# Kernel optimization log

Measured on AMD Instinct MI355X. Metric: run time of the kernel, lower is better.

Reference implementation:

```python
import jax, jax.numpy as jnp
import numpy as np

N_NODES = 100000


def _sage_conv(x, src, dst, w_l, b_l, w_r):
    # PyG SAGEConv (mean aggr): out = lin_l(mean_{j in N(i)} x_j) + lin_r(x_i)
    msg = x[src]                                   # [E, d] gather
    agg = jax.ops.segment_sum(msg, dst, num_segments=N_NODES)   # [N, d]
    deg = jax.ops.segment_sum(jnp.ones_like(dst, dtype=x.dtype), dst,
                              num_segments=N_NODES)             # [N]
    mean = agg / jnp.maximum(deg, 1.0)[:, None]
    return mean @ w_l.T + b_l + x @ w_r.T


def setup_inputs() -> dict:
    key = jax.random.key(0)
    ks = jax.random.split(key, 8)
    in_dim, hid, out_dim = 128, 128, 64
    n_edges = 1600000
    x = jax.random.normal(ks[0], (N_NODES, in_dim), dtype=jnp.float32)
    edge_index = jax.random.randint(ks[1], (2, n_edges), 0, N_NODES, dtype=jnp.int64)
    s1 = 1.0 / np.sqrt(in_dim)
    s2 = 1.0 / np.sqrt(hid)
    w1_l = jax.random.uniform(ks[2], (hid, in_dim), jnp.float32, -s1, s1)
    b1 = jax.random.uniform(ks[3], (hid,), jnp.float32, -s1, s1)
    w1_r = jax.random.uniform(ks[4], (hid, in_dim), jnp.float32, -s1, s1)
    w2_l = jax.random.uniform(ks[5], (out_dim, hid), jnp.float32, -s2, s2)
    b2 = jax.random.uniform(ks[6], (out_dim,), jnp.float32, -s2, s2)
    w2_r = jax.random.uniform(ks[7], (out_dim, hid), jnp.float32, -s2, s2)
    return {"x": x, "edge_index": edge_index, "w1_l": w1_l, "b1": b1,
            "w1_r": w1_r, "w2_l": w2_l, "b2": b2, "w2_r": w2_r}


def reference(x, edge_index, w1_l, b1, w1_r, w2_l, b2, w2_r):
    src, dst = edge_index[0], edge_index[1]
    h = _sage_conv(x, src, dst, w1_l, b1, w1_r)    # [N, hid]
    h = jax.nn.relu(h)
    out = _sage_conv(h, src, dst, w2_l, b2, w2_r)  # [N, out_dim]
    return out
```

## Files before the change

### kernel.cpp

```cpp
#include <hip/hip_runtime.h>


namespace {
constexpr int NN   = 100000;
constexpr int NE   = 1600000;
constexpr int NBKT = 391;
constexpr int PB   = 256;
constexpr int CE   = NE / PB;

constexpr size_t W_BKT  = 0;
constexpr size_t W_BASE = 400;
constexpr size_t W_BCUR = 800;
constexpr size_t W_OFF  = 1200;
constexpr size_t W_PART = 101616;
constexpr size_t W_CSR  = 1701616;
constexpr size_t W_B1   = 3301616;
constexpr size_t W_B2   = 3318000;
constexpr size_t W_XQ   = 3326192;
constexpr size_t W_XR   = 6526192;
constexpr size_t W_H    = 12926192;
constexpr size_t W_HL   = 19326192;
constexpr size_t W_HR   = 22526192;
}

using short8  = __attribute__((ext_vector_type(8)))  short;
using f32x16  = __attribute__((ext_vector_type(16))) float;
using floatx2 = __attribute__((ext_vector_type(2)))  float;

__device__ inline unsigned short f2b(float f) {
  unsigned u = __builtin_bit_cast(unsigned, f);
  u = (u + 0x7fffu + ((u >> 16) & 1u)) >> 16;
  return (unsigned short)u;
}
__device__ inline float b2f_lo(unsigned u) { return __builtin_bit_cast(float, u << 16); }
__device__ inline float b2f_hi(unsigned u) { return __builtin_bit_cast(float, u & 0xffff0000u); }
__device__ inline float b2f(unsigned short s) { return __builtin_bit_cast(float, ((unsigned)s) << 16); }


__global__ __launch_bounds__(256) void prebucket_k(const int* __restrict__ dst,
                                                   int* __restrict__ bktCnt) {
  __shared__ int h[NBKT];
  int t = threadIdx.x;
  for (int j = t; j < NBKT; j += 256) h[j] = 0;
  __syncthreads();
  const int base = blockIdx.x * CE;
  for (int i = t; i < CE; i += 256) atomicAdd(&h[dst[base + i] >> 8], 1);
  __syncthreads();
  for (int j = t; j < NBKT; j += 256) if (h[j]) atomicAdd(&bktCnt[j], h[j]);
}

__global__ __launch_bounds__(512) void scanb_k(const int* __restrict__ bktCnt,
                                               int* __restrict__ bktBase,
                                               int* __restrict__ bktCur) {
  __shared__ int s[512];
  int t = threadIdx.x;
  int v = (t < NBKT) ? bktCnt[t] : 0;
  s[t] = v;
  __syncthreads();
  #pragma unroll
  for (int d = 1; d < 512; d <<= 1) {
    int u = (t >= d) ? s[t - d] : 0;
    __syncthreads();
    s[t] += u;
    __syncthreads();
  }
  int excl = s[t] - v;
  if (t <= NBKT) bktBase[t] = excl;
  if (t < NBKT)  bktCur[t]  = excl;
}

__global__ __launch_bounds__(256) void partition_k(const int* __restrict__ src,
                                                   const int* __restrict__ dst,
                                                   int* __restrict__ bktCur,
                                                   int* __restrict__ part) {
  __shared__ int  hist[NBKT + 1];
  __shared__ int  lo[NBKT + 1];
  __shared__ int  cur[NBKT + 1];
  __shared__ int  gb[NBKT + 1];
  __shared__ int  sh[256];
  __shared__ int  stage[CE];
  __shared__ unsigned short sbkt[CE];
  int t = threadIdx.x;
  const int base = blockIdx.x * CE;

  for (int j = t; j < NBKT + 1; j += 256) hist[j] = 0;
  __syncthreads();
  for (int i = t; i < CE; i += 256) atomicAdd(&hist[dst[base + i] >> 8], 1);
  __syncthreads();

  int j0 = 2 * t, j1 = 2 * t + 1;
  int h0 = (j0 < NBKT) ? hist[j0] : 0;
  int h1 = (j1 < NBKT) ? hist[j1] : 0;
  int ps = h0 + h1;
  sh[t] = ps;
  __syncthreads();
  #pragma unroll
  for (int d = 1; d < 256; d <<= 1) {
    int u = (t >= d) ? sh[t - d] : 0;
    __syncthreads();
    sh[t] += u;
    __syncthreads();
  }
  int e0 = sh[t] - ps;
  if (j0 < NBKT + 1) { lo[j0] = e0; cur[j0] = e0; }
  if (j1 < NBKT + 1) { lo[j1] = e0 + h0; cur[j1] = e0 + h0; }
  __syncthreads();

  for (int i = t; i < CE; i += 256) {
    int d = dst[base + i], s = src[base + i];
    int b = d >> 8;
    int p = atomicAdd(&cur[b], 1);
    stage[p] = ((d & 255) << 23) | s;
    sbkt[p]  = (unsigned short)b;
  }
  __syncthreads();

  for (int j = t; j < NBKT; j += 256)
    gb[j] = hist[j] ? atomicAdd(&bktCur[j], hist[j]) : 0;
  __syncthreads();

  for (int i = t; i < CE; i += 256) {
    int b = sbkt[i];
    part[gb[b] + (i - lo[b])] = stage[i];
  }
}

__global__ __launch_bounds__(256) void cfill_k(const int* __restrict__ part,
                                               const int* __restrict__ bktBase,
                                               int* __restrict__ off,
                                               int* __restrict__ csr) {
  __shared__ int cnt[256];
  __shared__ int cur[256];
  __shared__ int sh[256];
  int t = threadIdx.x;
  const int b = blockIdx.x;
  const int beg = bktBase[b], end = bktBase[b + 1];

  cnt[t] = 0;
  __syncthreads();
  for (int i = beg + t; i < end; i += 256)
    atomicAdd(&cnt[((unsigned)part[i]) >> 23], 1);
  __syncthreads();

  int v = cnt[t];
  sh[t] = v;
  __syncthreads();
  #pragma unroll
  for (int d = 1; d < 256; d <<= 1) {
    int u = (t >= d) ? sh[t - d] : 0;
    __syncthreads();
    sh[t] += u;
    __syncthreads();
  }
  int excl = sh[t] - v;
  off[b * 256 + t] = beg + excl;
  cur[t] = excl;
  __syncthreads();

  for (int i = beg + t; i < end; i += 256) {
    int w = part[i];
    int j = ((unsigned)w) >> 23;
    int p = atomicAdd(&cur[j], 1);
    csr[beg + p] = w & 0x7FFFFF;
  }
}


__global__ void prep_b_k(const float* __restrict__ w1l, const float* __restrict__ w1r,
                         const float* __restrict__ w2l, const float* __restrict__ w2r,
                         unsigned short* __restrict__ b1p, unsigned short* __restrict__ b2p) {
  int e = blockIdx.x * blockDim.x + threadIdx.x;
  if (e >= 6144) return;
  bool g2 = e >= 4096;
  int le = g2 ? e - 4096 : e;
  int nf = le >> 9, kk = (le >> 6) & 7, l = le & 63;
  int n = nf * 32 + (l & 31), half = l >> 5;
  const float* Wlo = g2 ? w2l : w1l;
  const float* Whi = g2 ? w2r : w1r;
  int split = g2 ? 64 : 128;
  unsigned short o[8];
  #pragma unroll
  for (int j = 0; j < 8; ++j) {
    int k = kk * 16 + ((j >= 4) ? 8 : 0) + half * 4 + (j & 3);
    float v = (n < split) ? Wlo[(size_t)n * 128 + k] : Whi[(size_t)(n - split) * 128 + k];
    o[j] = f2b(v);
  }
  unsigned short* dstp = (g2 ? b2p : b1p) + (size_t)le * 8;
  *(short8*)dstp = __builtin_bit_cast(short8, *(const ulonglong2*)o);
}


template<int NCOLS, bool AFP32, int MODE>
__global__ __launch_bounds__(512, 2) void gemm_k(const void* __restrict__ Aptr, int M,
                                                 const unsigned short* __restrict__ Bpack,
                                                 void* __restrict__ Cv,
                                                 void* __restrict__ C2v) {
  constexpr int NF = NCOLS / 64;
  __shared__ unsigned short As[128 * 128];
  const int t  = threadIdx.x;
  const int m0 = blockIdx.x * 128;

  #pragma unroll
  for (int i = 0; i < 4; ++i) {
    int G = t + 512 * i;
    int r = G >> 4, g = G & 15;
    int m = m0 + r;
    short8 v = {0, 0, 0, 0, 0, 0, 0, 0};
    if (AFP32) {
      if (m < M) {
        const float* p = (const float*)Aptr + (size_t)m * 128 + g * 8;
        float4 a = *(const float4*)p;
        float4 b = *(const float4*)(p + 4);
        v[0] = (short)f2b(a.x); v[1] = (short)f2b(a.y);
        v[2] = (short)f2b(a.z); v[3] = (short)f2b(a.w);
        v[4] = (short)f2b(b.x); v[5] = (short)f2b(b.y);
        v[6] = (short)f2b(b.z); v[7] = (short)f2b(b.w);
      }
    } else {
      if (m < M) v = *(const short8*)((const unsigned short*)Aptr + (size_t)m * 128 + g * 8);
    }
    *(short8*)(As + r * 128 + ((g ^ (r & 15)) << 3)) = v;
  }
  __syncthreads();

  const int wid = t >> 6, lane = t & 63;
  const int mw = wid >> 1, nw = wid & 1;
  const int m = mw * 32 + (lane & 31), half = lane >> 5;

  short8 af[8];
  #pragma unroll
  for (int kk = 0; kk < 8; ++kk) {
    const unsigned* p0 = (const unsigned*)(As + m * 128 + (((2 * kk)     ^ (m & 15)) << 3) + half * 4);
    const unsigned* p1 = (const unsigned*)(As + m * 128 + (((2 * kk + 1) ^ (m & 15)) << 3) + half * 4);
    uint4 comb = make_uint4(p0[0], p0[1], p1[0], p1[1]);
    af[kk] = __builtin_bit_cast(short8, comb);
  }

  #pragma unroll
  for (int nf = 0; nf < NF; ++nf) {
    const int nfg = nw * NF + nf;
    f32x16 acc;
    #pragma unroll
    for (int i = 0; i < 16; ++i) acc[i] = 0.f;
    #pragma unroll
    for (int kk = 0; kk < 8; ++kk) {
      short8 bf = *(const short8*)(Bpack + ((size_t)((nfg * 8 + kk) * 64 + lane)) * 8);
      acc = __builtin_amdgcn_mfma_f32_32x32x16_bf16(af[kk], bf, acc, 0, 0, 0);
    }
    const int col = nfg * 32 + (lane & 31);
    #pragma unroll
    for (int q = 0; q < 4; ++q)
      #pragma unroll
      for (int rr = 0; rr < 4; ++rr) {
        int row = rr + 8 * q + 4 * half;
        int mo  = m0 + mw * 32 + row;
        if (mo < M) {
          float v = acc[q * 4 + rr];
          if (MODE == 1) {
            if (col < 128) {
              int p8 = __builtin_amdgcn_cvt_pk_fp8_f32(v, v, 0, false);
              ((unsigned char*)C2v)[(size_t)mo * 128 + col] = (unsigned char)(p8 & 0xff);
            } else {
              ((unsigned short*)Cv)[(size_t)mo * 128 + (col - 128)] = f2b(v);
            }
          } else {
            if (col < 64) {
              int p8 = __builtin_amdgcn_cvt_pk_fp8_f32(v, v, 0, false);
              ((unsigned char*)Cv)[(size_t)mo * 64 + col] = (unsigned char)(p8 & 0xff);
            } else {
              ((unsigned short*)C2v)[(size_t)mo * 64 + (col - 64)] = f2b(v);
            }
          }
        }
      }
  }
}


__global__ __launch_bounds__(256) void agg1_k(const unsigned char* __restrict__ xq,
                                              const unsigned short* __restrict__ xr,
                                              const int* __restrict__ off,
                                              const int* __restrict__ csr,
                                              const float* __restrict__ b1,
                                              unsigned short* __restrict__ h) {
  int wid  = (blockIdx.x * blockDim.x + threadIdx.x) >> 6;
  int lane = threadIdx.x & 63;
  if (wid >= NN) return;
  const int g = lane >> 4, sub = lane & 15;
  int s0 = off[wid], s1 = off[wid + 1];

  float acc[8];
  #pragma unroll
  for (int k = 0; k < 8; ++k) acc[k] = 0.f;

  for (int e = s0; e < s1; e += 16) {
    int e0 = e + g, e1 = e + 4 + g, e2 = e + 8 + g, e3 = e + 12 + g;
    uint2 v0 = make_uint2(0u, 0u), v1 = make_uint2(0u, 0u);
    uint2 v2 = make_uint2(0u, 0u), v3 = make_uint2(0u, 0u);
    if (e0 < s1) v0 = *(const uint2*)(xq + (size_t)csr[e0] * 128 + sub * 8);
    if (e1 < s1) v1 = *(const uint2*)(xq + (size_t)csr[e1] * 128 + sub * 8);
    if (e2 < s1) v2 = *(const uint2*)(xq + (size_t)csr[e2] * 128 + sub * 8);
    if (e3 < s1) v3 = *(const uint2*)(xq + (size_t)csr[e3] * 128 + sub * 8);
    floatx2 f;
    f = __builtin_amdgcn_cvt_pk_f32_fp8(v0.x, false); acc[0] += f.x; acc[1] += f.y;
    f = __builtin_amdgcn_cvt_pk_f32_fp8(v0.x, true);  acc[2] += f.x; acc[3] += f.y;
    f = __builtin_amdgcn_cvt_pk_f32_fp8(v0.y, false); acc[4] += f.x; acc[5] += f.y;
    f = __builtin_amdgcn_cvt_pk_f32_fp8(v0.y, true);  acc[6] += f.x; acc[7] += f.y;
    f = __builtin_amdgcn_cvt_pk_f32_fp8(v1.x, false); acc[0] += f.x; acc[1] += f.y;
    f = __builtin_amdgcn_cvt_pk_f32_fp8(v1.x, true);  acc[2] += f.x; acc[3] += f.y;
    f = __builtin_amdgcn_cvt_pk_f32_fp8(v1.y, false); acc[4] += f.x; acc[5] += f.y;
    f = __builtin_amdgcn_cvt_pk_f32_fp8(v1.y, true);  acc[6] += f.x; acc[7] += f.y;
    f = __builtin_amdgcn_cvt_pk_f32_fp8(v2.x, false); acc[0] += f.x; acc[1] += f.y;
    f = __builtin_amdgcn_cvt_pk_f32_fp8(v2.x, true);  acc[2] += f.x; acc[3] += f.y;
    f = __builtin_amdgcn_cvt_pk_f32_fp8(v2.y, false); acc[4] += f.x; acc[5] += f.y;
    f = __builtin_amdgcn_cvt_pk_f32_fp8(v2.y, true);  acc[6] += f.x; acc[7] += f.y;
    f = __builtin_amdgcn_cvt_pk_f32_fp8(v3.x, false); acc[0] += f.x; acc[1] += f.y;
    f = __builtin_amdgcn_cvt_pk_f32_fp8(v3.x, true);  acc[2] += f.x; acc[3] += f.y;
    f = __builtin_amdgcn_cvt_pk_f32_fp8(v3.y, false); acc[4] += f.x; acc[5] += f.y;
    f = __builtin_amdgcn_cvt_pk_f32_fp8(v3.y, true);  acc[6] += f.x; acc[7] += f.y;
  }

  #pragma unroll
  for (int k = 0; k < 8; ++k) {
    acc[k] += __shfl_xor(acc[k], 16);
    acc[k] += __shfl_xor(acc[k], 32);
  }

  float inv = 1.f / fmaxf((float)(s1 - s0), 1.f);
  int widx = sub * 4 + g;
  unsigned su = ((const unsigned*)xr)[(size_t)wid * 64 + widx];
  float2 bb = *(const float2*)(b1 + 2 * widx);
  float h0 = fmaxf(fmaf(acc[2 * g],     inv, bb.x + b2f_lo(su)), 0.f);
  float h1 = fmaxf(fmaf(acc[2 * g + 1], inv, bb.y + b2f_hi(su)), 0.f);
  unsigned packed = (unsigned)f2b(h0) | ((unsigned)f2b(h1) << 16);
  ((unsigned*)h)[(size_t)wid * 64 + widx] = packed;
}


__global__ __launch_bounds__(256) void agg2_k(const unsigned char* __restrict__ hl,
                                              const unsigned short* __restrict__ hr,
                                              const int* __restrict__ off,
                                              const int* __restrict__ csr,
                                              const float* __restrict__ b2,
                                              float* __restrict__ out) {
  int wid  = (blockIdx.x * blockDim.x + threadIdx.x) >> 6;
  int lane = threadIdx.x & 63;
  if (wid >= NN) return;
  const int g = lane >> 4, sub = lane & 15;
  int s0 = off[wid], s1 = off[wid + 1];

  float acc[4];
  #pragma unroll
  for (int k = 0; k < 4; ++k) acc[k] = 0.f;

  for (int e = s0; e < s1; e += 16) {
    int e0 = e + g, e1 = e + 4 + g, e2 = e + 8 + g, e3 = e + 12 + g;
    unsigned v0 = 0u, v1 = 0u, v2 = 0u, v3 = 0u;
    if (e0 < s1) v0 = *(const unsigned*)(hl + (size_t)csr[e0] * 64 + sub * 4);
    if (e1 < s1) v1 = *(const unsigned*)(hl + (size_t)csr[e1] * 64 + sub * 4);
    if (e2 < s1) v2 = *(const unsigned*)(hl + (size_t)csr[e2] * 64 + sub * 4);
    if (e3 < s1) v3 = *(const unsigned*)(hl + (size_t)csr[e3] * 64 + sub * 4);
    floatx2 f;
    f = __builtin_amdgcn_cvt_pk_f32_fp8(v0, false); acc[0] += f.x; acc[1] += f.y;
    f = __builtin_amdgcn_cvt_pk_f32_fp8(v0, true);  acc[2] += f.x; acc[3] += f.y;
    f = __builtin_amdgcn_cvt_pk_f32_fp8(v1, false); acc[0] += f.x; acc[1] += f.y;
    f = __builtin_amdgcn_cvt_pk_f32_fp8(v1, true);  acc[2] += f.x; acc[3] += f.y;
    f = __builtin_amdgcn_cvt_pk_f32_fp8(v2, false); acc[0] += f.x; acc[1] += f.y;
    f = __builtin_amdgcn_cvt_pk_f32_fp8(v2, true);  acc[2] += f.x; acc[3] += f.y;
    f = __builtin_amdgcn_cvt_pk_f32_fp8(v3, false); acc[0] += f.x; acc[1] += f.y;
    f = __builtin_amdgcn_cvt_pk_f32_fp8(v3, true);  acc[2] += f.x; acc[3] += f.y;
  }

  #pragma unroll
  for (int k = 0; k < 4; ++k) {
    acc[k] += __shfl_xor(acc[k], 16);
    acc[k] += __shfl_xor(acc[k], 32);
  }

  float inv = 1.f / fmaxf((float)(s1 - s0), 1.f);
  int c = sub * 4 + g;
  float r = b2f(hr[(size_t)wid * 64 + c]);
  out[(size_t)wid * 64 + c] = fmaf(acc[g], inv, b2[c] + r);
}


extern "C" void kernel_launch(void* const* d_in, const int* in_sizes, int n_in,
                              void* d_out, int out_size, void* d_ws, size_t ws_size,
                              hipStream_t stream) {
  const float* x   = (const float*)d_in[0];
  const int*   ei  = (const int*)d_in[1];
  const float* w1l = (const float*)d_in[2];
  const float* b1  = (const float*)d_in[3];
  const float* w1r = (const float*)d_in[4];
  const float* w2l = (const float*)d_in[5];
  const float* b2  = (const float*)d_in[6];
  const float* w2r = (const float*)d_in[7];
  float* out = (float*)d_out;

  const int* src = ei;
  const int* dst = ei + NE;

  int* bktCnt  = (int*)d_ws + W_BKT;
  int* bktBase = (int*)d_ws + W_BASE;
  int* bktCur  = (int*)d_ws + W_BCUR;
  int* off     = (int*)d_ws + W_OFF;
  int* part    = (int*)d_ws + W_PART;
  int* csr     = (int*)d_ws + W_CSR;
  unsigned short* b1p = (unsigned short*)((int*)d_ws + W_B1);
  unsigned short* b2p = (unsigned short*)((int*)d_ws + W_B2);
  unsigned char*  xq  = (unsigned char*)((int*)d_ws + W_XQ);
  unsigned short* xr  = (unsigned short*)((int*)d_ws + W_XR);
  unsigned short* h   = (unsigned short*)((int*)d_ws + W_H);
  unsigned char*  hl  = (unsigned char*)((int*)d_ws + W_HL);
  unsigned short* hr  = (unsigned short*)((int*)d_ws + W_HR);

  hipMemsetAsync(bktCnt, 0, 400 * 4, stream);

  prebucket_k<<<PB, 256, 0, stream>>>(dst, bktCnt);
  scanb_k<<<1, 512, 0, stream>>>(bktCnt, bktBase, bktCur);
  partition_k<<<PB, 256, 0, stream>>>(src, dst, bktCur, part);
  cfill_k<<<NBKT, 256, 0, stream>>>(part, bktBase, off, csr);
  prep_b_k<<<24, 256, 0, stream>>>(w1l, w1r, w2l, w2r, b1p, b2p);

  const int gb = (NN + 127) / 128;

  gemm_k<256, true, 1><<<gb, 512, 0, stream>>>((const void*)x, NN, b1p, xr, xq);

  agg1_k<<<(NN * 64 + 255) / 256, 256, 0, stream>>>(xq, xr, off, csr, b1, h);

  gemm_k<128, false, 2><<<gb, 512, 0, stream>>>((const void*)h, NN, b2p, hl, hr);

  agg2_k<<<(NN * 64 + 255) / 256, 256, 0, stream>>>(hl, hr, off, csr, b2, out);
}
```

Before: 208.8 us.

## Split layer-1 fp8 features into two column halves aggregated by separate kernels

The first GEMM now writes the fp8 neighbor-projected features as two separate 64-column arrays instead of one 128-byte row. Layer-1 aggregation runs as two kernel launches, one per half. Each gathers 4 bytes per lane with 8 edges in flight per lane, and only half the lanes write output. The aim is to shrink each pass's gather working set (6.4 MB per half) so it fits better in cache and raises memory-level parallelism. The cost is reading the CSR indices twice, an extra launch, and gathering 4-byte words instead of 8-byte ones.

Measured after the change: 239.4 us. 14.7% more time.

```diff
diff --git a/kernel.cpp b/kernel.cpp
--- a/kernel.cpp
+++ b/kernel.cpp
@@ -16,11 +16,12 @@
 constexpr size_t W_CSR  = 1701616;
 constexpr size_t W_B1   = 3301616;
 constexpr size_t W_B2   = 3318000;
-constexpr size_t W_XQ   = 3326192;
+constexpr size_t W_XQA  = 3326192;
+constexpr size_t W_XQB  = 4926192;
 constexpr size_t W_XR   = 6526192;
 constexpr size_t W_H    = 12926192;
 constexpr size_t W_HL   = 19326192;
-constexpr size_t W_HR   = 22526192;
+constexpr size_t W_HR   = 20926192;
 }
 
 using short8  = __attribute__((ext_vector_type(8)))  short;
@@ -194,7 +195,8 @@
 __global__ __launch_bounds__(512, 2) void gemm_k(const void* __restrict__ Aptr, int M,
                                                  const unsigned short* __restrict__ Bpack,
                                                  void* __restrict__ Cv,
-                                                 void* __restrict__ C2v) {
+                                                 void* __restrict__ C2v,
+                                                 void* __restrict__ C3v) {
   constexpr int NF = NCOLS / 64;
   __shared__ unsigned short As[128 * 128];
   const int t  = threadIdx.x;
@@ -257,9 +259,12 @@
         if (mo < M) {
           float v = acc[q * 4 + rr];
           if (MODE == 1) {
-            if (col < 128) {
+            if (col < 64) {
               int p8 = __builtin_amdgcn_cvt_pk_fp8_f32(v, v, 0, false);
-              ((unsigned char*)C2v)[(size_t)mo * 128 + col] = (unsigned char)(p8 & 0xff);
+              ((unsigned char*)C2v)[(size_t)mo * 64 + col] = (unsigned char)(p8 & 0xff);
+            } else if (col < 128) {
+              int p8 = __builtin_amdgcn_cvt_pk_fp8_f32(v, v, 0, false);
+              ((unsigned char*)C3v)[(size_t)mo * 64 + (col - 64)] = (unsigned char)(p8 & 0xff);
             } else {
               ((unsigned short*)Cv)[(size_t)mo * 128 + (col - 128)] = f2b(v);
             }
@@ -277,63 +282,55 @@
 }
 
 
-__global__ __launch_bounds__(256) void agg1_k(const unsigned char* __restrict__ xq,
-                                              const unsigned short* __restrict__ xr,
-                                              const int* __restrict__ off,
-                                              const int* __restrict__ csr,
-                                              const float* __restrict__ b1,
-                                              unsigned short* __restrict__ h) {
+template<int HALF>
+__global__ __launch_bounds__(256) void agg1h_k(const unsigned char* __restrict__ xqH,
+                                               const unsigned short* __restrict__ xr,
+                                               const int* __restrict__ off,
+                                               const int* __restrict__ csr,
+                                               const float* __restrict__ b1,
+                                               unsigned short* __restrict__ h) {
   int wid  = (blockIdx.x * blockDim.x + threadIdx.x) >> 6;
   int lane = threadIdx.x & 63;
   if (wid >= NN) return;
   const int g = lane >> 4, sub = lane & 15;
   int s0 = off[wid], s1 = off[wid + 1];
 
-  float acc[8];
-  #pragma unroll
-  for (int k = 0; k < 8; ++k) acc[k] = 0.f;
-
-  for (int e = s0; e < s1; e += 16) {
-    int e0 = e + g, e1 = e + 4 + g, e2 = e + 8 + g, e3 = e + 12 + g;
-    uint2 v0 = make_uint2(0u, 0u), v1 = make_uint2(0u, 0u);
-    uint2 v2 = make_uint2(0u, 0u), v3 = make_uint2(0u, 0u);
-    if (e0 < s1) v0 = *(const uint2*)(xq + (size_t)csr[e0] * 128 + sub * 8);
-    if (e1 < s1) v1 = *(const uint2*)(xq + (size_t)csr[e1] * 128 + sub * 8);
-    if (e2 < s1) v2 = *(const uint2*)(xq + (size_t)csr[e2] * 128 + sub * 8);
-    if (e3 < s1) v3 = *(const uint2*)(xq + (size_t)csr[e3] * 128 + sub * 8);
-    floatx2 f;
-    f = __builtin_amdgcn_cvt_pk_f32_fp8(v0.x, false); acc[0] += f.x; acc[1] += f.y;
-    f = __builtin_amdgcn_cvt_pk_f32_fp8(v0.x, true);  acc[2] += f.x; acc[3] += f.y;
-    f = __builtin_amdgcn_cvt_pk_f32_fp8(v0.y, false); acc[4] += f.x; acc[5] += f.y;
-    f = __builtin_amdgcn_cvt_pk_f32_fp8(v0.y, true);  acc[6] += f.x; acc[7] += f.y;
-    f = __builtin_amdgcn_cvt_pk_f32_fp8(v1.x, false); acc[0] += f.x; acc[1] += f.y;
-    f = __builtin_amdgcn_cvt_pk_f32_fp8(v1.x, true);  acc[2] += f.x; acc[3] += f.y;
-    f = __builtin_amdgcn_cvt_pk_f32_fp8(v1.y, false); acc[4] += f.x; acc[5] += f.y;
-    f = __builtin_amdgcn_cvt_pk_f32_fp8(v1.y, true);  acc[6] += f.x; acc[7] += f.y;
-    f = __builtin_amdgcn_cvt_pk_f32_fp8(v2.x, false); acc[0] += f.x; acc[1] += f.y;
-    f = __builtin_amdgcn_cvt_pk_f32_fp8(v2.x, true);  acc[2] += f.x; acc[3] += f.y;
-    f = __builtin_amdgcn_cvt_pk_f32_fp8(v2.y, false); acc[4] += f.x; acc[5] += f.y;
-    f = __builtin_amdgcn_cvt_pk_f32_fp8(v2.y, true);  acc[6] += f.x; acc[7] += f.y;
-    f = __builtin_amdgcn_cvt_pk_f32_fp8(v3.x, false); acc[0] += f.x; acc[1] += f.y;
-    f = __builtin_amdgcn_cvt_pk_f32_fp8(v3.x, true);  acc[2] += f.x; acc[3] += f.y;
-    f = __builtin_amdgcn_cvt_pk_f32_fp8(v3.y, false); acc[4] += f.x; acc[5] += f.y;
-    f = __builtin_amdgcn_cvt_pk_f32_fp8(v3.y, true);  acc[6] += f.x; acc[7] += f.y;
-  }
-
-  #pragma unroll
-  for (int k = 0; k < 8; ++k) {
+  float acc[4];
+  #pragma unroll
+  for (int k = 0; k < 4; ++k) acc[k] = 0.f;
+
+  for (int e = s0; e < s1; e += 32) {
+    unsigned v[8];
+    #pragma unroll
+    for (int k = 0; k < 8; ++k) {
+      int ee = e + 4 * k + g;
+      v[k] = 0u;
+      if (ee < s1) v[k] = *(const unsigned*)(xqH + (size_t)csr[ee] * 64 + sub * 4);
+    }
+    #pragma unroll
+    for (int k = 0; k < 8; ++k) {
+      floatx2 f;
+      f = __builtin_amdgcn_cvt_pk_f32_fp8(v[k], false); acc[0] += f.x; acc[1] += f.y;
+      f = __builtin_amdgcn_cvt_pk_f32_fp8(v[k], true);  acc[2] += f.x; acc[3] += f.y;
+    }
+  }
+
+  #pragma unroll
+  for (int k = 0; k < 4; ++k) {
     acc[k] += __shfl_xor(acc[k], 16);
     acc[k] += __shfl_xor(acc[k], 32);
   }
 
-  float inv = 1.f / fmaxf((float)(s1 - s0), 1.f);
-  int widx = sub * 4 + g;
-  unsigned su = ((const unsigned*)xr)[(size_t)wid * 64 + widx];
-  float2 bb = *(const float2*)(b1 + 2 * widx);
-  float h0 = fmaxf(fmaf(acc[2 * g],     inv, bb.x + b2f_lo(su)), 0.f);
-  float h1 = fmaxf(fmaf(acc[2 * g + 1], inv, bb.y + b2f_hi(su)), 0.f);
-  unsigned packed = (unsigned)f2b(h0) | ((unsigned)f2b(h1) << 16);
-  ((unsigned*)h)[(size_t)wid * 64 + widx] = packed;
+  if (g < 2) {
+    float inv = 1.f / fmaxf((float)(s1 - s0), 1.f);
+    int w  = sub * 2 + g;
+    int gw = wid * 64 + HALF * 32 + w;
+    unsigned su = ((const unsigned*)xr)[gw];
+    float2 bb = *(const float2*)(b1 + 2 * (HALF * 32 + w));
+    float h0 = fmaxf(fmaf(acc[2 * g],     inv, bb.x + b2f_lo(su)), 0.f);
+    float h1 = fmaxf(fmaf(acc[2 * g + 1], inv, bb.y + b2f_hi(su)), 0.f);
+    ((unsigned*)h)[gw] = (unsigned)f2b(h0) | ((unsigned)f2b(h1) << 16);
+  }
 }
 
 
@@ -408,7 +405,8 @@
   int* csr     = (int*)d_ws + W_CSR;
   unsigned short* b1p = (unsigned short*)((int*)d_ws + W_B1);
   unsigned short* b2p = (unsigned short*)((int*)d_ws + W_B2);
-  unsigned char*  xq  = (unsigned char*)((int*)d_ws + W_XQ);
+  unsigned char*  xqA = (unsigned char*)((int*)d_ws + W_XQA);
+  unsigned char*  xqB = (unsigned char*)((int*)d_ws + W_XQB);
   unsigned short* xr  = (unsigned short*)((int*)d_ws + W_XR);
   unsigned short* h   = (unsigned short*)((int*)d_ws + W_H);
   unsigned char*  hl  = (unsigned char*)((int*)d_ws + W_HL);
@@ -423,12 +421,14 @@
   prep_b_k<<<24, 256, 0, stream>>>(w1l, w1r, w2l, w2r, b1p, b2p);
 
   const int gb = (NN + 127) / 128;
-
-  gemm_k<256, true, 1><<<gb, 512, 0, stream>>>((const void*)x, NN, b1p, xr, xq);
-
-  agg1_k<<<(NN * 64 + 255) / 256, 256, 0, stream>>>(xq, xr, off, csr, b1, h);
-
-  gemm_k<128, false, 2><<<gb, 512, 0, stream>>>((const void*)h, NN, b2p, hl, hr);
-
-  agg2_k<<<(NN * 64 + 255) / 256, 256, 0, stream>>>(hl, hr, off, csr, b2, out);
-}
+  const int ab = (NN * 64 + 255) / 256;
+
+  gemm_k<256, true, 1><<<gb, 512, 0, stream>>>((const void*)x, NN, b1p, xr, xqA, xqB);
+
+  agg1h_k<0><<<ab, 256, 0, stream>>>(xqA, xr, off, csr, b1, h);
+  agg1h_k<1><<<ab, 256, 0, stream>>>(xqB, xr, off, csr, b1, h);
+
+  gemm_k<128, false, 2><<<gb, 512, 0, stream>>>((const void*)h, NN, b2p, hl, hr, nullptr);
+
+  agg2_k<<<ab, 256, 0, stream>>>(hl, hr, off, csr, b2, out);
+}
```
